# Kernel tuning notes

Hardware: AMD Instinct MI355X
Metric: run time of the kernel (lower is better)

The kernel has to match this reference:

```python
import jax, jax.numpy as jnp
import numpy as np

N = 50000          # nodes
E = 1_600_000      # edges (avg degree 32)
F_IN, H1, H2 = 512, 128, 64


def setup_inputs() -> dict:
    key = jax.random.key(0)
    ks = jax.random.split(key, 9)
    x = jax.random.normal(ks[0], (N, F_IN), jnp.float32)
    edge_index = jax.random.randint(ks[1], (2, E), 0, N, jnp.int32)
    # Glorot-ish scaled weights
    W1 = jax.random.normal(ks[2], (F_IN, H1), jnp.float32) / np.sqrt(F_IN)
    b1 = jnp.zeros((H1,), jnp.float32)
    W2 = jax.random.normal(ks[3], (H1, H2), jnp.float32) / np.sqrt(H1)
    b2 = jnp.zeros((H2,), jnp.float32)
    W3 = jax.random.normal(ks[4], (H1, H2), jnp.float32) / np.sqrt(H1)
    b3 = jnp.zeros((H2,), jnp.float32)
    eps = jax.random.normal(ks[5], (N, H2), jnp.float32)
    return {"x": x, "edge_index": edge_index, "W1": W1, "b1": b1,
            "W2": W2, "b2": b2, "W3": W3, "b3": b3, "eps": eps}


def _gcn_norm(edge_index, n, dtype):
    # add self loops, then symmetric normalization deg^-1/2 A_hat deg^-1/2
    loop = jnp.arange(n, dtype=edge_index.dtype)
    src = jnp.concatenate([edge_index[0], loop])
    dst = jnp.concatenate([edge_index[1], loop])
    deg = jax.ops.segment_sum(jnp.ones_like(dst, dtype=dtype), dst, num_segments=n)
    dinv = jax.lax.rsqrt(jnp.maximum(deg, 1.0))
    norm = dinv[src] * dinv[dst]          # [E + N]
    return src, dst, norm


def _gcn_conv(h, src, dst, norm, W, b):
    hw = h @ W                             # dense linear transform [N, out]
    msg = hw[src] * norm[:, None]          # gather + scale      [E+N, out]
    return jax.ops.segment_sum(msg, dst, num_segments=h.shape[0]) + b


def reference(x, edge_index, W1, b1, W2, b2, W3, b3, eps):
    src, dst, norm = _gcn_norm(edge_index, x.shape[0], x.dtype)
    h1 = _gcn_conv(x, src, dst, norm, W1, b1)      # gc1
    mu = _gcn_conv(h1, src, dst, norm, W2, b2)     # gc2
    logvar = _gcn_conv(h1, src, dst, norm, W3, b3) # gc3
    # faithful to source: std = exp(logvar), z = eps*std + mu (training path)
    z = eps * jnp.exp(logvar) + mu
    return z
```

## Files before the change

kernel.cpp:

```cpp
#include <hip/hip_runtime.h>
#include <math.h>

#define NN   50000
#define NE   1600000
#define FIN  512
#define H1F  128
#define NBUK  391
#define BIN_EPB 4096
#define NBIN  391

typedef __attribute__((ext_vector_type(8))) short bf16x8;
typedef __attribute__((ext_vector_type(4))) float f32x4;
typedef __attribute__((ext_vector_type(2))) float f32x2;

__device__ __forceinline__ float bflo(unsigned v) { return __uint_as_float(v << 16); }
__device__ __forceinline__ float bfhi(unsigned v) { return __uint_as_float(v & 0xffff0000u); }
__device__ __forceinline__ unsigned short f2bf(float f) {
  unsigned u = __float_as_uint(f);
  u += 0x7fffu + ((u >> 16) & 1u);
  return (unsigned short)(u >> 16);
}
__device__ __forceinline__ unsigned pack2bf(float a, float b) {
  return (unsigned)f2bf(a) | ((unsigned)f2bf(b) << 16);
}

#if defined(__has_builtin)
#  if __has_builtin(__builtin_amdgcn_cvt_pk_f32_fp8) && __has_builtin(__builtin_amdgcn_cvt_pk_fp8_f32)
#    define HW_FP8 1
#  endif
#endif
#ifndef HW_FP8
#  define HW_FP8 0
#endif

__device__ __forceinline__ float fp8dec_sw(unsigned v, int sh) {
  unsigned b = (v >> sh) & 0xffu;
  unsigned bits = ((b & 0x80u) << 24) | ((b & 0x7fu) << 20);
  return __uint_as_float(bits) * 0x1.0p+120f;
}
__device__ __forceinline__ unsigned fp8enc_sw(float f) {
  unsigned u = __float_as_uint(f * 0x1.0p-120f);
  unsigned s = (u >> 24) & 0x80u;
  u &= 0x7fffffffu;
  u += 0x7ffffu + ((u >> 20) & 1u);
  unsigned e = u >> 20;
  if (e > 0x7fu) e = 0x7fu;
  return s | e;
}

__device__ __forceinline__ void fp8dec4(unsigned v, float& a, float& b, float& c, float& d) {
#if HW_FP8
  f32x2 lo = __builtin_amdgcn_cvt_pk_f32_fp8(v, false);
  f32x2 hi = __builtin_amdgcn_cvt_pk_f32_fp8(v, true);
  a = lo[0]; b = lo[1]; c = hi[0]; d = hi[1];
#else
  a = fp8dec_sw(v, 0); b = fp8dec_sw(v, 8); c = fp8dec_sw(v, 16); d = fp8dec_sw(v, 24);
#endif
}
__device__ __forceinline__ unsigned fp8enc4(float a, float b, float c, float d) {
#if HW_FP8
  unsigned r = (unsigned)__builtin_amdgcn_cvt_pk_fp8_f32(a, b, 0, false);
  r = (unsigned)__builtin_amdgcn_cvt_pk_fp8_f32(c, d, (int)r, true);
  return r;
#else
  return fp8enc_sw(a) | (fp8enc_sw(b) << 8) | (fp8enc_sw(c) << 16) | (fp8enc_sw(d) << 24);
#endif
}


__global__ __launch_bounds__(256) void k_binhist(const int* __restrict__ ei,
                                                 int* __restrict__ gh) {
  __shared__ int hist[NBUK];
  int t  = threadIdx.x;
  int e0 = blockIdx.x * BIN_EPB;
  for (int b = t; b < NBUK; b += 256) hist[b] = 0;
  __syncthreads();
#pragma unroll
  for (int j = 0; j < 16; ++j) {
    int e = e0 + j * 256 + t;
    if (e < NE) atomicAdd(&hist[ei[NE + e] >> 7], 1);
  }
  __syncthreads();
  for (int b = t; b < NBUK; b += 256) gh[(size_t)b * NBIN + blockIdx.x] = hist[b];
}

__global__ __launch_bounds__(64) void k_rowscan(int* __restrict__ gh,
                                                int* __restrict__ btot) {
  int row  = blockIdx.x;
  int lane = threadIdx.x;
  int* g = gh + (size_t)row * NBIN;
  int carry = 0;
  for (int c = 0; c < (NBIN + 63) / 64; ++c) {
    int idx = c * 64 + lane;
    int v = (idx < NBIN) ? g[idx] : 0;
    int incl = v;
#pragma unroll
    for (int off = 1; off < 64; off <<= 1) {
      int u = __shfl_up(incl, off, 64);
      if (lane >= off) incl += u;
    }
    if (idx < NBIN) g[idx] = carry + (incl - v);
    carry += __shfl(incl, 63, 64);
  }
  if (lane == 0) btot[row] = carry;
}

__global__ __launch_bounds__(512) void k_bscan(const int* __restrict__ btot,
                                               int* __restrict__ bbase) {
  __shared__ int ts[512];
  int t = threadIdx.x;
  int v = (t < NBUK) ? btot[t] : 0;
  ts[t] = v;
  __syncthreads();
  for (int off = 1; off < 512; off <<= 1) {
    int val = ts[t];
    int add = (t >= off) ? ts[t - off] : 0;
    __syncthreads();
    ts[t] = val + add;
    __syncthreads();
  }
  if (t < NBUK) bbase[t] = ts[t] - v;
  if (t == NBUK - 1) bbase[NBUK] = ts[t];
}

__global__ __launch_bounds__(256) void k_binscat(const int* __restrict__ ei,
                                                 const int* __restrict__ gh,
                                                 const int* __restrict__ bbase,
                                                 unsigned* __restrict__ tmp) {
  __shared__ int hist[NBUK];
  __shared__ int sbase[NBUK];
  int t  = threadIdx.x;
  int e0 = blockIdx.x * BIN_EPB;
  for (int b = t; b < NBUK; b += 256) hist[b] = 0;
  __syncthreads();

  unsigned short d16[16];
  unsigned short p16[16];
#pragma unroll
  for (int j = 0; j < 16; ++j) {
    int e = e0 + j * 256 + t;
    d16[j] = 0xFFFFu;
    if (e < NE) {
      int d = ei[NE + e];
      d16[j] = (unsigned short)d;
      p16[j] = (unsigned short)atomicAdd(&hist[d >> 7], 1);
    }
  }
  __syncthreads();
  for (int b = t; b < NBUK; b += 256)
    sbase[b] = bbase[b] + gh[(size_t)b * NBIN + blockIdx.x];
  __syncthreads();
#pragma unroll
  for (int j = 0; j < 16; ++j) {
    int e = e0 + j * 256 + t;
    if (e < NE) {
      int s = ei[e];
      int d = (int)d16[j];
      tmp[sbase[d >> 7] + (int)p16[j]] = ((unsigned)s << 16) | (unsigned)d;
    }
  }
}

__global__ __launch_bounds__(256) void k_fill2x(const unsigned* __restrict__ tmp,
                                                const int* __restrict__ bbase,
                                                int* __restrict__ rowptr,
                                                float* __restrict__ dinv,
                                                int* __restrict__ csr) {
  __shared__ int cnt[128];
  __shared__ int lofs[128];
  __shared__ int cur[128];
  __shared__ int ts[256];
  int b  = blockIdx.x;
  int t  = threadIdx.x;
  int n0 = b << 7;
  int beg = bbase[b];
  int end = bbase[b + 1];
  if (t < 128) { cnt[t] = 0; cur[t] = 0; }
  __syncthreads();
  for (int i = beg + t; i < end; i += 256)
    atomicAdd(&cnt[tmp[i] & 127u], 1);
  __syncthreads();
  int v = (t < 128) ? cnt[t] : 0;
  ts[t] = v;
  __syncthreads();
  for (int off = 1; off < 128; off <<= 1) {
    int val = ts[t];
    int add = (t >= off) ? ts[t - off] : 0;
    __syncthreads();
    ts[t] = val + add;
    __syncthreads();
  }
  if (t < 128) {
    int excl = ts[t] - v;
    lofs[t] = beg + excl;
    int n = n0 + t;
    if (n < NN) {
      rowptr[n] = beg + excl;
      dinv[n]   = rsqrtf((float)(v + 1));
    }
  }
  if (b == NBUK - 1 && t == 0) rowptr[NN] = end;
  __syncthreads();
  for (int i = beg + t; i < end; i += 256) {
    unsigned pk = tmp[i];
    int dl = (int)(pk & 127u);
    int s  = (int)(pk >> 16);
    int p  = atomicAdd(&cur[dl], 1);
    csr[lofs[dl] + p] = s;
  }
}


__global__ __launch_bounds__(256) void k_cvtw1f(const float* __restrict__ W,
                                                unsigned short* __restrict__ W1f) {
  int i = blockIdx.x * 256 + threadIdx.x;
  if (i >= 16 * 8 * 64) return;
  int s = i >> 9, rem = i & 511, f = rem >> 6, lane = rem & 63;
  int row = f * 16 + (lane & 15);
  int kb  = s * 32 + (lane >> 4) * 8;
  unsigned short c8[8];
#pragma unroll
  for (int j = 0; j < 8; ++j) c8[j] = f2bf(W[(size_t)(kb + j) * H1F + row]);
  *(uint4*)&W1f[(size_t)i * 8] = *(uint4*)c8;
}

__global__ __launch_bounds__(256) void k_cvtw23f(const float* __restrict__ W2,
                                                 const float* __restrict__ W3,
                                                 unsigned short* __restrict__ Wf) {
  int i = blockIdx.x * 256 + threadIdx.x;
  if (i >= 4 * 8 * 64) return;
  int s = i >> 9, rem = i & 511, f = rem >> 6, lane = rem & 63;
  int row = f * 16 + (lane & 15);
  int kb  = s * 32 + (lane >> 4) * 8;
  const float* Wsrc = (row < 64) ? W2 : W3;
  int c = row & 63;
  unsigned short c8[8];
#pragma unroll
  for (int j = 0; j < 8; ++j) c8[j] = f2bf(Wsrc[(size_t)(kb + j) * 64 + c]);
  *(uint4*)&Wf[(size_t)i * 8] = *(uint4*)c8;
}


#define G1_ABUF 5120
#define G1_BBUF 8192
#define G1_BUF  (G1_ABUF + G1_BBUF)
#define G1_NSTEP 16

__global__ __launch_bounds__(256) void k_gemm1m(const float* __restrict__ X,
                                                const uint4* __restrict__ W1fv,
                                                unsigned* __restrict__ out8) {
  __shared__ char lds[2 * G1_BUF];
  int tid  = threadIdx.x;
  int row0 = blockIdx.x * 64;
  int w    = tid >> 6;
  int lane = tid & 63;

  int ar = tid >> 2, aq = tid & 3;

  float4 av0, av1;
  uint4  bu0, bu1;

  auto load_g = [&](int s) {
    int k0 = s * 32;
    int row = row0 + ar;
    av0 = make_float4(0.f, 0.f, 0.f, 0.f);
    av1 = av0;
    if (row < NN) {
      const float* gp = X + (size_t)row * FIN + k0 + aq * 8;
      av0 = *(const float4*)gp;
      av1 = *(const float4*)(gp + 4);
    }
    const uint4* bp = W1fv + (size_t)s * 512;
    bu0 = bp[tid];
    bu1 = bp[tid + 256];
  };
  auto store_l = [&](int buf) {
    char* Ab = lds + buf * G1_BUF;
    char* Bb = Ab + G1_ABUF;
    uint4 ap;
    ap.x = pack2bf(av0.x, av0.y); ap.y = pack2bf(av0.z, av0.w);
    ap.z = pack2bf(av1.x, av1.y); ap.w = pack2bf(av1.z, av1.w);
    *(uint4*)(Ab + ar * 80 + aq * 16) = ap;
    *(uint4*)(Bb + tid * 16)        = bu0;
    *(uint4*)(Bb + tid * 16 + 4096) = bu1;
  };

  f32x4 acc[8];
#pragma unroll
  for (int f = 0; f < 8; ++f) acc[f] = (f32x4){0.f, 0.f, 0.f, 0.f};

  load_g(0);
  store_l(0);

  for (int s = 0; s < G1_NSTEP; ++s) {
    if (s + 1 < G1_NSTEP) load_g(s + 1);
    __syncthreads();
    const char* Ab = lds + (s & 1) * G1_BUF;
    const char* Bb = Ab + G1_ABUF;
    bf16x8 xa = *(const bf16x8*)(Ab + (w * 16 + (lane & 15)) * 80 + (lane >> 4) * 16);
#pragma unroll
    for (int f = 0; f < 8; ++f) {
      bf16x8 bt = *(const bf16x8*)(Bb + f * 1024 + lane * 16);
      acc[f] = __builtin_amdgcn_mfma_f32_16x16x32_bf16(bt, xa, acc[f], 0, 0, 0);
    }
    if (s + 1 < G1_NSTEP) store_l((s + 1) & 1);
  }

  int orow = row0 + w * 16 + (lane & 15);
  if (orow < NN) {
    size_t base = (size_t)orow * 32;
#pragma unroll
    for (int f = 0; f < 8; ++f) {
      int col = f * 16 + (lane >> 4) * 4;
      out8[base + (col >> 2)] = fp8enc4(acc[f][0], acc[f][1], acc[f][2], acc[f][3]);
    }
  }
}


template<bool BIAS, bool OUTBF>
__global__ __launch_bounds__(256) void k_agg8(const unsigned* __restrict__ feat,
                                              const int* __restrict__ rowptr,
                                              const int* __restrict__ csr,
                                              const float* __restrict__ dinv,
                                              const float* __restrict__ bias,
                                              void* __restrict__ out) {
  int gw   = (blockIdx.x * 256 + threadIdx.x) >> 5;
  int lane = threadIdx.x & 31;
  if (gw >= NN) return;
  int beg = rowptr[gw], end = rowptr[gw + 1];
  float di = dinv[gw];
  float a0 = 0.f, a1 = 0.f, a2 = 0.f, a3 = 0.f;

  for (int e = beg; e < end; e += 32) {
    int cnt = end - e; if (cnt > 32) cnt = 32;
    int sv = 0; float wv = 0.f;
    if (lane < cnt) { sv = csr[e + lane]; wv = dinv[sv]; }
    int j = 0;
    for (; j + 8 <= cnt; j += 8) {
      float ww[8];
      unsigned vv[8];
#pragma unroll
      for (int q = 0; q < 8; ++q) {
        int s = __shfl(sv, j + q, 32);
        ww[q] = __shfl(wv, j + q, 32);
        vv[q] = feat[(size_t)s * 32 + lane];
      }
#pragma unroll
      for (int q = 0; q < 8; ++q) {
        float d0, d1, d2, d3;
        fp8dec4(vv[q], d0, d1, d2, d3);
        a0 += ww[q] * d0; a1 += ww[q] * d1; a2 += ww[q] * d2; a3 += ww[q] * d3;
      }
    }
    for (; j < cnt; ++j) {
      int s = __shfl(sv, j, 32);
      float w = __shfl(wv, j, 32);
      float d0, d1, d2, d3;
      fp8dec4(feat[(size_t)s * 32 + lane], d0, d1, d2, d3);
      a0 += w * d0; a1 += w * d1; a2 += w * d2; a3 += w * d3;
    }
  }
  {
    float d0, d1, d2, d3;
    fp8dec4(feat[(size_t)gw * 32 + lane], d0, d1, d2, d3);
    a0 = di * (a0 + di * d0);
    a1 = di * (a1 + di * d1);
    a2 = di * (a2 + di * d2);
    a3 = di * (a3 + di * d3);
  }
  if (BIAS) {
    float4 bb = *(const float4*)&bias[lane * 4];
    a0 += bb.x; a1 += bb.y; a2 += bb.z; a3 += bb.w;
  }
  if (OUTBF) {
    uint2 pk; pk.x = pack2bf(a0, a1); pk.y = pack2bf(a2, a3);
    *(uint2*)&((unsigned*)out)[(size_t)gw * 64 + lane * 2] = pk;
  } else {
    ((unsigned*)out)[(size_t)gw * 32 + lane] = fp8enc4(a0, a1, a2, a3);
  }
}


#define G2_ASTRIDE 272
#define G2_AOFF    (64 * G2_ASTRIDE)
#define G2_BBYTES  32768

__global__ __launch_bounds__(256) void k_gemm2m(const unsigned short* __restrict__ Gb,
                                                const uint4* __restrict__ W23fv,
                                                const float* __restrict__ b2,
                                                const float* __restrict__ b3,
                                                const float* __restrict__ eps,
                                                float* __restrict__ z) {
  __shared__ char lds[G2_AOFF + G2_BBYTES];
  int tid  = threadIdx.x;
  int row0 = blockIdx.x * 64;
  int w    = tid >> 6;
  int lane = tid & 63;

  {
    int ar = tid >> 2, aq = tid & 3;
    int row = row0 + ar;
    uint4 a0 = {}, a1 = {}, a2 = {}, a3 = {};
    if (row < NN) {
      const uint4* gp = (const uint4*)(Gb + (size_t)row * H1F) + aq * 4;
      a0 = gp[0]; a1 = gp[1]; a2 = gp[2]; a3 = gp[3];
    }
    char* Ab = lds + ar * G2_ASTRIDE + aq * 64;
    *(uint4*)(Ab)      = a0;
    *(uint4*)(Ab + 16) = a1;
    *(uint4*)(Ab + 32) = a2;
    *(uint4*)(Ab + 48) = a3;
  }
  {
    uint4* Bb = (uint4*)(lds + G2_AOFF);
#pragma unroll
    for (int j = 0; j < 8; ++j) Bb[tid + j * 256] = W23fv[tid + j * 256];
  }
  __syncthreads();

  f32x4 acc[8];
#pragma unroll
  for (int f = 0; f < 8; ++f) acc[f] = (f32x4){0.f, 0.f, 0.f, 0.f};

#pragma unroll
  for (int s = 0; s < 4; ++s) {
    bf16x8 xa = *(const bf16x8*)(lds + (w * 16 + (lane & 15)) * G2_ASTRIDE + s * 64 + (lane >> 4) * 16);
#pragma unroll
    for (int f = 0; f < 8; ++f) {
      bf16x8 bt = *(const bf16x8*)(lds + G2_AOFF + ((s * 512 + f * 64 + lane) << 4));
      acc[f] = __builtin_amdgcn_mfma_f32_16x16x32_bf16(bt, xa, acc[f], 0, 0, 0);
    }
  }

  int orow = row0 + w * 16 + (lane & 15);
  if (orow < NN) {
    int q = lane >> 4;
    size_t base = (size_t)orow * 64;
#pragma unroll
    for (int f = 0; f < 4; ++f) {
      int c = f * 16 + q * 4;
      float4 ev = *(const float4*)&eps[base + c];
      float4 zo;
      zo.x = ev.x * __expf(acc[f + 4][0] + b3[c + 0]) + acc[f][0] + b2[c + 0];
      zo.y = ev.y * __expf(acc[f + 4][1] + b3[c + 1]) + acc[f][1] + b2[c + 1];
      zo.z = ev.z * __expf(acc[f + 4][2] + b3[c + 2]) + acc[f][2] + b2[c + 2];
      zo.w = ev.w * __expf(acc[f + 4][3] + b3[c + 3]) + acc[f][3] + b2[c + 3];
      *(float4*)&z[base + c] = zo;
    }
  }
}


extern "C" void kernel_launch(void* const* d_in, const int* in_sizes, int n_in,
                              void* d_out, int out_size, void* d_ws, size_t ws_size,
                              hipStream_t stream) {
  const float* x   = (const float*)d_in[0];
  const int*   ei  = (const int*)  d_in[1];
  const float* W1  = (const float*)d_in[2];
  const float* b1  = (const float*)d_in[3];
  const float* W2  = (const float*)d_in[4];
  const float* b2  = (const float*)d_in[5];
  const float* W3  = (const float*)d_in[6];
  const float* b3  = (const float*)d_in[7];
  const float* eps = (const float*)d_in[8];
  float* z = (float*)d_out;

  char* ws = (char*)d_ws;
  size_t o = 0;
  auto alloc = [&](size_t bytes) -> void* {
    void* p = ws + o;
    o = (o + bytes + 255) & ~(size_t)255;
    return p;
  };
  int*   gh     = (int*)  alloc((size_t)NBUK * NBIN * 4);
  int*   btot   = (int*)  alloc((size_t)NBUK * 4);
  int*   bbase  = (int*)  alloc((size_t)(NBUK + 1) * 4);
  int*   rowptr = (int*)  alloc((size_t)(NN + 1) * 4);
  float* dinv   = (float*)alloc((size_t)NN * 4);
  int*   csr    = (int*)  alloc((size_t)NE * 4);
  unsigned* tmp = (unsigned*)alloc((size_t)NE * 4);
  unsigned short* W1f  = (unsigned short*)alloc((size_t)16 * 8 * 64 * 8 * 2);
  unsigned short* W23f = (unsigned short*)alloc((size_t)4 * 8 * 64 * 8 * 2);
  unsigned* hw8 = (unsigned*)alloc((size_t)NN * 32 * 4);
  unsigned* h8  = (unsigned*)alloc((size_t)NN * 32 * 4);
  unsigned short* gb = (unsigned short*)alloc((size_t)NN * H1F * 2);

  k_binhist<<<NBIN, 256, 0, stream>>>(ei, gh);
  k_rowscan<<<NBUK, 64, 0, stream>>>(gh, btot);
  k_bscan  <<<1, 512, 0, stream>>>(btot, bbase);
  k_binscat<<<NBIN, 256, 0, stream>>>(ei, gh, bbase, tmp);
  k_fill2x <<<NBUK, 256, 0, stream>>>(tmp, bbase, rowptr, dinv, csr);
  k_cvtw1f <<<32, 256, 0, stream>>>(W1, W1f);
  k_cvtw23f<<<8, 256, 0, stream>>>(W2, W3, W23f);

  k_gemm1m <<<(NN + 63) / 64, 256, 0, stream>>>(x, (const uint4*)W1f, hw8);
  k_agg8<true,  false><<<(NN * 32 + 255) / 256, 256, 0, stream>>>(hw8, rowptr, csr, dinv, b1, (void*)h8);
  k_agg8<false, true ><<<(NN * 32 + 255) / 256, 256, 0, stream>>>(h8,  rowptr, csr, dinv, nullptr, (void*)gb);
  k_gemm2m <<<(NN + 63) / 64, 256, 0, stream>>>(gb, (const uint4*)W23f, b2, b3, eps, z);
}
```

Measured before the change: 154.2 us.

## Pre-scale features by dinv in producers to drop per-edge weight gathers

The GEMM1 epilogue and the first aggregation's output now multiply each row by its own dinv before storing in fp8. The aggregation kernels can then sum neighbor features without weights, which removes the per-edge dinv[src] gather and its shuffle. The accumulation also moves to packed f32x2 adds spread over two accumulator sets to shorten dependency chains. The cost is an extra multiply in the producers. Scaling before fp8 quantization changes the rounding behaviour slightly.

```diff
diff --git a/kernel.cpp b/kernel.cpp
--- a/kernel.cpp
+++ b/kernel.cpp
@@ -48,13 +48,13 @@
   return s | e;
 }
 
-__device__ __forceinline__ void fp8dec4(unsigned v, float& a, float& b, float& c, float& d) {
+__device__ __forceinline__ void fp8dec4p(unsigned v, f32x2& lo, f32x2& hi) {
 #if HW_FP8
-  f32x2 lo = __builtin_amdgcn_cvt_pk_f32_fp8(v, false);
-  f32x2 hi = __builtin_amdgcn_cvt_pk_f32_fp8(v, true);
-  a = lo[0]; b = lo[1]; c = hi[0]; d = hi[1];
+  lo = __builtin_amdgcn_cvt_pk_f32_fp8(v, false);
+  hi = __builtin_amdgcn_cvt_pk_f32_fp8(v, true);
 #else
-  a = fp8dec_sw(v, 0); b = fp8dec_sw(v, 8); c = fp8dec_sw(v, 16); d = fp8dec_sw(v, 24);
+  lo = (f32x2){fp8dec_sw(v, 0), fp8dec_sw(v, 8)};
+  hi = (f32x2){fp8dec_sw(v, 16), fp8dec_sw(v, 24)};
 #endif
 }
 __device__ __forceinline__ unsigned fp8enc4(float a, float b, float c, float d) {
@@ -248,6 +248,7 @@
 
 __global__ __launch_bounds__(256) void k_gemm1m(const float* __restrict__ X,
                                                 const uint4* __restrict__ W1fv,
+                                                const float* __restrict__ dinv,
                                                 unsigned* __restrict__ out8) {
   __shared__ char lds[2 * G1_BUF];
   int tid  = threadIdx.x;
@@ -308,11 +309,13 @@
 
   int orow = row0 + w * 16 + (lane & 15);
   if (orow < NN) {
+    float di = dinv[orow];
     size_t base = (size_t)orow * 32;
 #pragma unroll
     for (int f = 0; f < 8; ++f) {
       int col = f * 16 + (lane >> 4) * 4;
-      out8[base + (col >> 2)] = fp8enc4(acc[f][0], acc[f][1], acc[f][2], acc[f][3]);
+      out8[base + (col >> 2)] = fp8enc4(di * acc[f][0], di * acc[f][1],
+                                        di * acc[f][2], di * acc[f][3]);
     }
   }
 }
@@ -330,45 +333,45 @@
   if (gw >= NN) return;
   int beg = rowptr[gw], end = rowptr[gw + 1];
   float di = dinv[gw];
-  float a0 = 0.f, a1 = 0.f, a2 = 0.f, a3 = 0.f;
+  f32x2 aA = (f32x2){0.f, 0.f}, bA = (f32x2){0.f, 0.f};
+  f32x2 aB = (f32x2){0.f, 0.f}, bB = (f32x2){0.f, 0.f};
 
   for (int e = beg; e < end; e += 32) {
     int cnt = end - e; if (cnt > 32) cnt = 32;
-    int sv = 0; float wv = 0.f;
-    if (lane < cnt) { sv = csr[e + lane]; wv = dinv[sv]; }
+    int sv = 0;
+    if (lane < cnt) sv = csr[e + lane];
     int j = 0;
     for (; j + 8 <= cnt; j += 8) {
-      float ww[8];
       unsigned vv[8];
 #pragma unroll
       for (int q = 0; q < 8; ++q) {
         int s = __shfl(sv, j + q, 32);
-        ww[q] = __shfl(wv, j + q, 32);
         vv[q] = feat[(size_t)s * 32 + lane];
       }
 #pragma unroll
       for (int q = 0; q < 8; ++q) {
-        float d0, d1, d2, d3;
-        fp8dec4(vv[q], d0, d1, d2, d3);
-        a0 += ww[q] * d0; a1 += ww[q] * d1; a2 += ww[q] * d2; a3 += ww[q] * d3;
+        f32x2 lo, hi;
+        fp8dec4p(vv[q], lo, hi);
+        if (q & 1) { aB += lo; bB += hi; }
+        else       { aA += lo; bA += hi; }
       }
     }
     for (; j < cnt; ++j) {
       int s = __shfl(sv, j, 32);
-      float w = __shfl(wv, j, 32);
-      float d0, d1, d2, d3;
-      fp8dec4(feat[(size_t)s * 32 + lane], d0, d1, d2, d3);
-      a0 += w * d0; a1 += w * d1; a2 += w * d2; a3 += w * d3;
+      f32x2 lo, hi;
+      fp8dec4p(feat[(size_t)s * 32 + lane], lo, hi);
+      aA += lo; bA += hi;
     }
   }
   {
-    float d0, d1, d2, d3;
-    fp8dec4(feat[(size_t)gw * 32 + lane], d0, d1, d2, d3);
-    a0 = di * (a0 + di * d0);
-    a1 = di * (a1 + di * d1);
-    a2 = di * (a2 + di * d2);
-    a3 = di * (a3 + di * d3);
-  }
+    f32x2 lo, hi;
+    fp8dec4p(feat[(size_t)gw * 32 + lane], lo, hi);
+    aA += lo; bA += hi;
+  }
+  f32x2 s01 = aA + aB;
+  f32x2 s23 = bA + bB;
+  float a0 = di * s01[0], a1 = di * s01[1];
+  float a2 = di * s23[0], a3 = di * s23[1];
   if (BIAS) {
     float4 bb = *(const float4*)&bias[lane * 4];
     a0 += bb.x; a1 += bb.y; a2 += bb.z; a3 += bb.w;
@@ -377,7 +380,7 @@
     uint2 pk; pk.x = pack2bf(a0, a1); pk.y = pack2bf(a2, a3);
     *(uint2*)&((unsigned*)out)[(size_t)gw * 64 + lane * 2] = pk;
   } else {
-    ((unsigned*)out)[(size_t)gw * 32 + lane] = fp8enc4(a0, a1, a2, a3);
+    ((unsigned*)out)[(size_t)gw * 32 + lane] = fp8enc4(di * a0, di * a1, di * a2, di * a3);
   }
 }
 
@@ -494,7 +497,7 @@
   k_cvtw1f <<<32, 256, 0, stream>>>(W1, W1f);
   k_cvtw23f<<<8, 256, 0, stream>>>(W2, W3, W23f);
 
-  k_gemm1m <<<(NN + 63) / 64, 256, 0, stream>>>(x, (const uint4*)W1f, hw8);
+  k_gemm1m <<<(NN + 63) / 64, 256, 0, stream>>>(x, (const uint4*)W1f, dinv, hw8);
   k_agg8<true,  false><<<(NN * 32 + 255) / 256, 256, 0, stream>>>(hw8, rowptr, csr, dinv, b1, (void*)h8);
   k_agg8<false, true ><<<(NN * 32 + 255) / 256, 256, 0, stream>>>(h8,  rowptr, csr, dinv, nullptr, (void*)gb);
   k_gemm2m <<<(NN + 63) / 64, 256, 0, stream>>>(gb, (const uint4*)W23f, b2, b3, eps, z);
```

After: 143.4 us. 7.0% less time.
